# Performance work log

Measured on AMD Instinct MI355X. Metric: run time of the kernel, lower is better.

Reference implementation:

```python
import jax, jax.numpy as jnp
import numpy as np

B, S, D = 4, 2048, 1024
H, DH = 16, 64

def setup_inputs() -> dict:
    key = jax.random.key(0)
    kx, kq, kk, kv, ko = jax.random.split(key, 5)
    scale = 1.0 / np.sqrt(D)
    return {
        "x": jax.random.normal(kx, (B, S, D), dtype=jnp.float32),
        "Wq": jax.random.normal(kq, (D, H * DH), dtype=jnp.float32) * scale,
        "Wk": jax.random.normal(kk, (D, H * DH), dtype=jnp.float32) * scale,
        "Wv": jax.random.normal(kv, (D, H * DH), dtype=jnp.float32) * scale,
        "Wo": jax.random.normal(ko, (H * DH, D), dtype=jnp.float32) * scale,
    }

def reference(x, Wq, Wk, Wv, Wo):
    b, s, _ = x.shape
    # projections -> [b, h, s, dh]
    q = (x @ Wq).reshape(b, s, H, DH).transpose(0, 2, 1, 3)
    k = (x @ Wk).reshape(b, s, H, DH).transpose(0, 2, 1, 3)
    v = (x @ Wv).reshape(b, s, H, DH).transpose(0, 2, 1, 3)
    logits = jnp.einsum("bhqd,bhkd->bhqk", q, k) / jnp.sqrt(jnp.float32(DH))
    # mask = triu(ones, diagonal=1): True above diagonal -> masked
    mask = jnp.triu(jnp.ones((s, s), dtype=bool), k=1)
    logits = jnp.where(mask, -jnp.inf, logits)
    probs = jax.nn.softmax(logits, axis=-1)
    attn = jnp.einsum("bhqk,bhkd->bhqd", probs, v)
    attn = attn.transpose(0, 2, 1, 3).reshape(b, s, H * DH)
    return attn @ Wo
```

## Files before the change

kernel.cpp:

```cpp
#include <hip/hip_runtime.h>
#include <stdint.h>

#define NB 4
#define NS 2048
#define ND 1024
#define NH 16
#define NDH 64

typedef __attribute__((ext_vector_type(8))) short bf16x8;
typedef __attribute__((ext_vector_type(4))) float f32x4;
typedef __attribute__((ext_vector_type(2))) unsigned int u32x2;

#define MFMA16(a, b, c) __builtin_amdgcn_mfma_f32_16x16x32_bf16((a), (b), (c), 0, 0, 0)

__device__ __forceinline__ uint16_t f2bf(float f) {
  uint32_t u = __builtin_bit_cast(uint32_t, f);
  return (uint16_t)((u + 0x7FFFu + ((u >> 16) & 1u)) >> 16);
}

__device__ __forceinline__ uint32_t pk2(float lo, float hi) {
  return (__builtin_bit_cast(uint32_t, hi) & 0xFFFF0000u) |
         (__builtin_bit_cast(uint32_t, lo) >> 16);
}

__device__ __forceinline__ void gload_lds16(const void* g, void* l) {
  __builtin_amdgcn_global_load_lds(
      (const __attribute__((address_space(1))) uint32_t*)(uintptr_t)g,
      (__attribute__((address_space(3))) uint32_t*)(uintptr_t)l, 16, 0, 0);
}

__global__ __launch_bounds__(256) void cvt_bf16_kernel(const float* __restrict__ src,
                                                       uint16_t* __restrict__ dst, int n4) {
  int i = blockIdx.x * 256 + threadIdx.x;
  if (i >= n4) return;
  const float4 f = *(const float4*)(src + (size_t)i * 4);
  union { uint16_t u[4]; uint64_t q; } o;
  o.u[0] = f2bf(f.x); o.u[1] = f2bf(f.y); o.u[2] = f2bf(f.z); o.u[3] = f2bf(f.w);
  *(uint64_t*)(dst + (size_t)i * 4) = o.q;
}

__global__ __launch_bounds__(256) void transpose_cvt(const float* __restrict__ W,
                                                     uint16_t* __restrict__ Wt) {
  __shared__ uint16_t tile[32][33];
  const int bx = blockIdx.x * 32;
  const int by = blockIdx.y * 32;
  const int tx = threadIdx.x;
  const int ty = threadIdx.y;
#pragma unroll
  for (int j = 0; j < 4; j++)
    tile[ty + j * 8][tx] = f2bf(W[(size_t)(by + ty + j * 8) * 1024 + bx + tx]);
  __syncthreads();
#pragma unroll
  for (int j = 0; j < 4; j++)
    Wt[(size_t)(bx + ty + j * 8) * 1024 + by + tx] = tile[tx][ty + j * 8];
}

template <int MODE, int NBX>
__global__ __launch_bounds__(256) void gemm_bt(const uint16_t* __restrict__ A,
                                               const uint16_t* __restrict__ Bt,
                                               uint16_t* __restrict__ O0,
                                               uint16_t* __restrict__ O1,
                                               uint16_t* __restrict__ O2,
                                               float* __restrict__ OF) {
  __shared__ uint16_t lds[2][128 * 32];
  const int tid = threadIdx.x;
  const int lane = tid & 63;
  const int wave = tid >> 6;
  const int wr = wave >> 1, wc = wave & 1;
  const int l15 = lane & 15, lg = lane >> 4;

  const int nwg = NBX * 64;
  const int wg = ((int)blockIdx.x & 7) * (nwg >> 3) + ((int)blockIdx.x >> 3);
  const int st = wg >> 5, in32 = wg & 31;
  const int sy = in32 >> 2, sx = in32 & 3;
  const int stx = st % (NBX / 4), sty = st / (NBX / 4);
  const int row0 = (sty * 8 + sy) * 128;
  const int col0 = (stx * 4 + sx) * 128;

  f32x4 acc[4][4];
#pragma unroll
  for (int i = 0; i < 4; i++)
#pragma unroll
    for (int j = 0; j < 4; j++) acc[i][j] = f32x4{0.f, 0.f, 0.f, 0.f};

  const int srow = tid >> 2;
  const int scb = (tid & 3) * 16;
  const char* Ab = (const char*)A;
  const char* Bb = (const char*)Bt;
  char* ldsA = (char*)&lds[0][0];
  char* ldsB = (char*)&lds[1][0];
  const int wbase = wave * 1024;

  for (int kt = 0; kt < 1024; kt += 32) {
#pragma unroll
    for (int j = 0; j < 2; ++j) {
      const int r = j * 64 + srow;
      gload_lds16(Ab + ((size_t)(row0 + r) * 1024 + kt) * 2 + scb, ldsA + j * 4096 + wbase);
      gload_lds16(Bb + ((size_t)(col0 + r) * 1024 + kt) * 2 + scb, ldsB + j * 4096 + wbase);
    }
    __syncthreads();
    bf16x8 bfr[4];
#pragma unroll
    for (int ni = 0; ni < 4; ni++)
      bfr[ni] = *(const bf16x8*)&lds[1][(wc * 64 + ni * 16 + l15) * 32 + lg * 8];
#pragma unroll
    for (int mi = 0; mi < 4; mi++) {
      const bf16x8 afr = *(const bf16x8*)&lds[0][(wr * 64 + mi * 16 + l15) * 32 + lg * 8];
#pragma unroll
      for (int ni = 0; ni < 4; ni++) acc[mi][ni] = MFMA16(afr, bfr[ni], acc[mi][ni]);
    }
    __syncthreads();
  }

#pragma unroll
  for (int mi = 0; mi < 4; mi++) {
#pragma unroll
    for (int ni = 0; ni < 4; ni++) {
      const int c = col0 + wc * 64 + ni * 16 + l15;
      const int rbase = row0 + wr * 64 + mi * 16 + lg * 4;
#pragma unroll
      for (int i = 0; i < 4; i++) {
        const int r = rbase + i;
        const float v = acc[mi][ni][i];
        if (MODE == 0) {
          const int which = c >> 10, cc = c & 1023;
          const int h = cc >> 6, dh = cc & 63;
          const int b = r >> 11, s = r & 2047;
          const size_t hb = (size_t)(b * NH + h);
          if (which == 0)
            O0[(hb * NS + s) * 64 + dh] = f2bf(v * 0.18033688011112042f);
          else if (which == 1)
            O1[(hb * NS + s) * 64 + dh] = f2bf(v);
          else
            O2[(((hb * 32 + (s >> 6)) * 64 + dh) * 64) + (s & 63)] = f2bf(v);
        } else {
          OF[(size_t)r * 1024 + c] = v;
        }
      }
    }
  }
}

__device__ __forceinline__ void stage_kv(const char* __restrict__ Kg,
                                         const char* __restrict__ Vg,
                                         char* kl, char* vl, int lane) {
#pragma unroll
  for (int j = 0; j < 8; ++j) {
    const int y = j * 1024 + lane * 16;
    const int r = y >> 7;
    const int zs = (r << 7) | ((((y >> 4) - r) & 7) << 4);
    gload_lds16(Kg + zs, kl + j * 1024);
    gload_lds16(Vg + zs, vl + j * 1024);
  }
}

__device__ __forceinline__ void attn_unit(const uint16_t* __restrict__ Qh,
                                          const char* __restrict__ Kg,
                                          const char* __restrict__ Vg,
                                          uint16_t* __restrict__ Aout,
                                          int b, int h, int gp, int l15, int lg, int lane,
                                          char* kl, char* vl,
                                          uint16_t (*pX)[64][16]) {
  const int qbA = gp * 32;
  const int qbB = qbA + 16;
  const int tmax = gp >> 1;
  const int nfdA = (2 * gp) & 3;
  const int nfdB = nfdA + 1;

  stage_kv(Kg, Vg, kl, vl, lane);

  const bf16x8 qfA0 = *(const bf16x8*)&Qh[(size_t)(qbA + l15) * 64 + lg * 8];
  const bf16x8 qfA1 = *(const bf16x8*)&Qh[(size_t)(qbA + l15) * 64 + 32 + lg * 8];
  const bf16x8 qfB0 = *(const bf16x8*)&Qh[(size_t)(qbB + l15) * 64 + lg * 8];
  const bf16x8 qfB1 = *(const bf16x8*)&Qh[(size_t)(qbB + l15) * 64 + 32 + lg * 8];

  const short one_bf = (short)0x3F80;
  const bf16x8 ones = {one_bf, one_bf, one_bf, one_bf, one_bf, one_bf, one_bf, one_bf};

  const int rsw = l15 & 7;

  const int wcol = ((lg + (l15 >> 2)) & 3) * 4;
  const int rr = l15 >> 2, cc0 = l15 & 3;
  const int rot = (2 * lg) & 3;
  const uint32_t pb = (uint32_t)(uintptr_t)&pX[0][0][0];
  const uint32_t addr0 = pb + (uint32_t)(lg * 256 + rr * 32 + (((cc0 + rot) & 3) * 8));
  const uint32_t addr1 = pb + (uint32_t)(lg * 256 + 128 + rr * 32 + (((cc0 + rot + 1) & 3) * 8));

  f32x4 oA[4], oB[4];
  f32x4 rsA = f32x4{0.f, 0.f, 0.f, 0.f};
  f32x4 rsB = f32x4{0.f, 0.f, 0.f, 0.f};
#pragma unroll
  for (int i = 0; i < 4; i++) {
    oA[i] = f32x4{0.f, 0.f, 0.f, 0.f};
    oB[i] = f32x4{0.f, 0.f, 0.f, 0.f};
  }

  for (int t = 0; t <= tmax; ++t) {
    asm volatile("s_waitcnt vmcnt(0)" ::: "memory");
    __builtin_amdgcn_sched_barrier(0);
    bf16x8 kf[4][2], vf[4][2];
#pragma unroll
    for (int nf = 0; nf < 4; ++nf)
#pragma unroll
      for (int kk = 0; kk < 2; ++kk) {
        const int off = (nf * 16 + l15) * 128 + (((kk * 4 + lg) + rsw) & 7) * 16;
        kf[nf][kk] = *(const bf16x8*)(kl + off);
        vf[nf][kk] = *(const bf16x8*)(vl + off);
      }
    asm volatile("s_waitcnt lgkmcnt(0)" ::: "memory");
    __builtin_amdgcn_sched_barrier(0);
    if (t < tmax) stage_kv(Kg + (size_t)(t + 1) * 8192, Vg + (size_t)(t + 1) * 8192, kl, vl, lane);

    const int nfmA = (t == tmax) ? nfdA : 3;
    const int nfmB = (t == tmax) ? nfdB : 3;
#pragma unroll
    for (int nf = 0; nf < 4; ++nf) {
      if (nf <= nfmB) {
        f32x4 a = f32x4{0.f, 0.f, 0.f, 0.f};
        a = MFMA16(qfB0, kf[nf][0], a);
        a = MFMA16(qfB1, kf[nf][1], a);
        if (t == tmax && nf == nfdB) {
#pragma unroll
          for (int i = 0; i < 4; i++)
            if (l15 > lg * 4 + i) a[i] = -1e30f;
        }
        {
          const float e0 = exp2f(a[0]), e1 = exp2f(a[1]);
          const float e2 = exp2f(a[2]), e3 = exp2f(a[3]);
          *(uint64_t*)&pX[1][nf * 16 + l15][wcol] =
              ((uint64_t)pk2(e2, e3) << 32) | pk2(e0, e1);
        }
        if (nf <= nfmA) {
          f32x4 c = f32x4{0.f, 0.f, 0.f, 0.f};
          c = MFMA16(qfA0, kf[nf][0], c);
          c = MFMA16(qfA1, kf[nf][1], c);
          if (t == tmax && nf == nfdA) {
#pragma unroll
            for (int i = 0; i < 4; i++)
              if (l15 > lg * 4 + i) c[i] = -1e30f;
          }
          const float e0 = exp2f(c[0]), e1 = exp2f(c[1]);
          const float e2 = exp2f(c[2]), e3 = exp2f(c[3]);
          *(uint64_t*)&pX[0][nf * 16 + l15][wcol] =
              ((uint64_t)pk2(e2, e3) << 32) | pk2(e0, e1);
        } else {
          *(uint64_t*)&pX[0][nf * 16 + l15][wcol] = 0ull;
        }
      } else {
        *(uint64_t*)&pX[0][nf * 16 + l15][wcol] = 0ull;
        *(uint64_t*)&pX[1][nf * 16 + l15][wcol] = 0ull;
      }
    }
    u32x2 a0, a1, a2, a3, b0, b1, b2, b3;
    asm volatile(
        "ds_read_b64_tr_b16 %0, %8\n\t"
        "ds_read_b64_tr_b16 %1, %9\n\t"
        "ds_read_b64_tr_b16 %2, %8 offset:1024\n\t"
        "ds_read_b64_tr_b16 %3, %9 offset:1024\n\t"
        "ds_read_b64_tr_b16 %4, %8 offset:2048\n\t"
        "ds_read_b64_tr_b16 %5, %9 offset:2048\n\t"
        "ds_read_b64_tr_b16 %6, %8 offset:3072\n\t"
        "ds_read_b64_tr_b16 %7, %9 offset:3072\n\t"
        "s_waitcnt lgkmcnt(0)"
        : "=&v"(a0), "=&v"(a1), "=&v"(a2), "=&v"(a3),
          "=&v"(b0), "=&v"(b1), "=&v"(b2), "=&v"(b3)
        : "v"(addr0), "v"(addr1)
        : "memory");
    union { u32x2 u2[2]; bf16x8 v8; } uA0, uA1, uB0, uB1;
    uA0.u2[0] = a0; uA0.u2[1] = a1;
    uA1.u2[0] = a2; uA1.u2[1] = a3;
    uB0.u2[0] = b0; uB0.u2[1] = b1;
    uB1.u2[0] = b2; uB1.u2[1] = b3;
    const bf16x8 paA0 = uA0.v8, paA1 = uA1.v8;
    const bf16x8 paB0 = uB0.v8, paB1 = uB1.v8;
    rsA = MFMA16(paA0, ones, rsA);
    rsA = MFMA16(paA1, ones, rsA);
    rsB = MFMA16(paB0, ones, rsB);
    rsB = MFMA16(paB1, ones, rsB);
#pragma unroll
    for (int df = 0; df < 4; ++df) {
      oA[df] = MFMA16(paA0, vf[df][0], oA[df]);
      oA[df] = MFMA16(paA1, vf[df][1], oA[df]);
      oB[df] = MFMA16(paB0, vf[df][0], oB[df]);
      oB[df] = MFMA16(paB1, vf[df][1], oB[df]);
    }
  }

#pragma unroll
  for (int df = 0; df < 4; ++df) {
#pragma unroll
    for (int i = 0; i < 4; i++) {
      const int qA = qbA + lg * 4 + i;
      const int qB = qbB + lg * 4 + i;
      Aout[((size_t)(b * NS + qA)) * 1024 + h * 64 + df * 16 + l15] = f2bf(oA[df][i] / rsA[i]);
      Aout[((size_t)(b * NS + qB)) * 1024 + h * 64 + df * 16 + l15] = f2bf(oB[df][i] / rsB[i]);
    }
  }
}

__global__ __launch_bounds__(256) void attn_fwd(const uint16_t* __restrict__ Q,
                                                const uint16_t* __restrict__ K,
                                                const uint16_t* __restrict__ Vt,
                                                uint16_t* __restrict__ Aout) {
  const int bid = blockIdx.x;
  const int xcd = bid & 7;
  const int sp = (bid >> 3) & 3;
  const int gblk = bid >> 5;

  const int w = threadIdx.x >> 6;
  const int lane = threadIdx.x & 63;
  const int l15 = lane & 15, lg = lane >> 4;
  const int g = gblk * 4 + w;

  __shared__ __align__(16) uint16_t plds[4][2][64][16];
  __shared__ __align__(16) char kstage[4][8192];
  __shared__ __align__(16) char vstage[4][8192];

  for (int seg = 0; seg < 2; ++seg) {
    const int slot = sp * 2 + seg;
    const int bh = (slot << 3) | xcd;
    const int gp = seg ? (63 - g) : g;
    const uint16_t* Qh = Q + (size_t)bh * (NS * 64);
    const char* Kg = (const char*)(K + (size_t)bh * (NS * 64));
    const char* Vg = (const char*)(Vt + (size_t)bh * (32 * 64 * 64));
    attn_unit(Qh, Kg, Vg, Aout, bh >> 4, bh & 15, gp, l15, lg, lane,
              kstage[w], vstage[w], plds[w]);
  }
}

extern "C" void kernel_launch(void* const* d_in, const int* in_sizes, int n_in,
                              void* d_out, int out_size, void* d_ws, size_t ws_size,
                              hipStream_t stream) {
  const float* x = (const float*)d_in[0];
  const float* Wq = (const float*)d_in[1];
  const float* Wk = (const float*)d_in[2];
  const float* Wv = (const float*)d_in[3];
  const float* Wo = (const float*)d_in[4];
  float* out = (float*)d_out;

  char* ws = (char*)d_ws;
  uint16_t* xb = (uint16_t*)(ws);
  uint16_t* Wt3 = (uint16_t*)(ws + (16u << 20));
  uint16_t* Wot = (uint16_t*)(ws + (22u << 20));
  uint16_t* Qb = (uint16_t*)(ws + (24u << 20));
  uint16_t* Kb = (uint16_t*)(ws + (40u << 20));
  uint16_t* Vt = (uint16_t*)(ws + (56u << 20));
  uint16_t* attn = xb;

  cvt_bf16_kernel<<<8192, 256, 0, stream>>>(x, xb, (NB * NS * ND) / 4);
  dim3 tb(32, 8);
  transpose_cvt<<<dim3(32, 32), tb, 0, stream>>>(Wq, Wt3);
  transpose_cvt<<<dim3(32, 32), tb, 0, stream>>>(Wk, Wt3 + (1u << 20));
  transpose_cvt<<<dim3(32, 32), tb, 0, stream>>>(Wv, Wt3 + (2u << 20));
  transpose_cvt<<<dim3(32, 32), tb, 0, stream>>>(Wo, Wot);

  gemm_bt<0, 24><<<1536, 256, 0, stream>>>(xb, Wt3, Qb, Kb, Vt, nullptr);
  attn_fwd<<<512, 256, 0, stream>>>(Qb, Kb, Vt, attn);
  gemm_bt<1, 8><<<512, 256, 0, stream>>>(attn, Wot, nullptr, nullptr, nullptr, out);
}
```

Baseline: 196.4 us.

## Double-buffer GEMM LDS tiles with K=64 steps and swizzled layout

Rewrites the projection GEMM main loop to use K-tiles of 64 instead of 32 and double-buffers the LDS tiles, so global-to-LDS loads for the next tile are issued before computing on the current one. Each iteration needs only one barrier instead of two, and the staged layout is XOR-style rotated by row to avoid LDS bank conflicts on the fragment reads. LDS use grows fourfold (64 KB per block), which may cut occupancy, and the tile loads now depend on the async load completing before the barrier.

```diff
diff --git a/kernel.cpp b/kernel.cpp
--- a/kernel.cpp
+++ b/kernel.cpp
@@ -62,7 +62,7 @@
                                                uint16_t* __restrict__ O1,
                                                uint16_t* __restrict__ O2,
                                                float* __restrict__ OF) {
-  __shared__ uint16_t lds[2][128 * 32];
+  __shared__ uint16_t lds[2][2][128 * 64];
   const int tid = threadIdx.x;
   const int lane = tid & 63;
   const int wave = tid >> 6;
@@ -83,34 +83,62 @@
 #pragma unroll
     for (int j = 0; j < 4; j++) acc[i][j] = f32x4{0.f, 0.f, 0.f, 0.f};
 
-  const int srow = tid >> 2;
-  const int scb = (tid & 3) * 16;
-  const char* Ab = (const char*)A;
-  const char* Bb = (const char*)Bt;
-  char* ldsA = (char*)&lds[0][0];
-  char* ldsB = (char*)&lds[1][0];
-  const int wbase = wave * 1024;
-
-  for (int kt = 0; kt < 1024; kt += 32) {
-#pragma unroll
-    for (int j = 0; j < 2; ++j) {
-      const int r = j * 64 + srow;
-      gload_lds16(Ab + ((size_t)(row0 + r) * 1024 + kt) * 2 + scb, ldsA + j * 4096 + wbase);
-      gload_lds16(Bb + ((size_t)(col0 + r) * 1024 + kt) * 2 + scb, ldsB + j * 4096 + wbase);
-    }
+  const char* Ag = (const char*)A + (size_t)row0 * 2048;
+  const char* Bg = (const char*)Bt + (size_t)col0 * 2048;
+
+  const int srr = tid >> 3;
+  const int csrc = ((tid & 7) - srr) & 7;
+  uint16_t* ldsA0 = &lds[0][0][0];
+
+#define STAGE_TILE(buf, t)                                                          \
+  {                                                                                 \
+    char* la = (char*)&lds[buf][0][0] + wave * 1024;                                \
+    char* lb = (char*)&lds[buf][1][0] + wave * 1024;                                \
+    _Pragma("unroll") for (int j = 0; j < 4; ++j) {                                 \
+      const size_t off = (size_t)(j * 32 + srr) * 2048 + (size_t)(t) * 128 + csrc * 16; \
+      gload_lds16(Ag + off, la + j * 4096);                                         \
+      gload_lds16(Bg + off, lb + j * 4096);                                         \
+    }                                                                               \
+  }
+
+  STAGE_TILE(0, 0);
+  __syncthreads();
+
+  int cur = 0;
+  for (int t = 0; t < 16; ++t) {
+    if (t < 15) STAGE_TILE(cur ^ 1, t + 1);
+    const char* cA = (const char*)&lds[cur][0][0];
+    const char* cB = (const char*)&lds[cur][1][0];
+    bf16x8 af[4][2], bfr[4][2];
+#pragma unroll
+    for (int mi = 0; mi < 4; mi++) {
+      const int row = wr * 64 + mi * 16 + l15;
+#pragma unroll
+      for (int ks = 0; ks < 2; ks++) {
+        const int ch = (ks * 4 + lg + (l15 & 7)) & 7;
+        af[mi][ks] = *(const bf16x8*)(cA + row * 128 + ch * 16);
+      }
+    }
+#pragma unroll
+    for (int ni = 0; ni < 4; ni++) {
+      const int row = wc * 64 + ni * 16 + l15;
+#pragma unroll
+      for (int ks = 0; ks < 2; ks++) {
+        const int ch = (ks * 4 + lg + (l15 & 7)) & 7;
+        bfr[ni][ks] = *(const bf16x8*)(cB + row * 128 + ch * 16);
+      }
+    }
+#pragma unroll
+    for (int ks = 0; ks < 2; ks++)
+#pragma unroll
+      for (int mi = 0; mi < 4; mi++)
+#pragma unroll
+        for (int ni = 0; ni < 4; ni++)
+          acc[mi][ni] = MFMA16(af[mi][ks], bfr[ni][ks], acc[mi][ni]);
     __syncthreads();
-    bf16x8 bfr[4];
-#pragma unroll
-    for (int ni = 0; ni < 4; ni++)
-      bfr[ni] = *(const bf16x8*)&lds[1][(wc * 64 + ni * 16 + l15) * 32 + lg * 8];
-#pragma unroll
-    for (int mi = 0; mi < 4; mi++) {
-      const bf16x8 afr = *(const bf16x8*)&lds[0][(wr * 64 + mi * 16 + l15) * 32 + lg * 8];
-#pragma unroll
-      for (int ni = 0; ni < 4; ni++) acc[mi][ni] = MFMA16(afr, bfr[ni], acc[mi][ni]);
-    }
-    __syncthreads();
-  }
+    cur ^= 1;
+  }
+  (void)ldsA0;
 
 #pragma unroll
   for (int mi = 0; mi < 4; mi++) {
@@ -139,6 +167,7 @@
       }
     }
   }
+#undef STAGE_TILE
 }
 
 __device__ __forceinline__ void stage_kv(const char* __restrict__ Kg,
```

After: 196.0 us. Within noise of the previous version (-0.2%).
